# Performance work log

Measured on AMD Instinct MI355X. Metric: run time of the kernel, lower is better.

The kernel has to match this reference:

```python
import jax, jax.numpy as jnp
import numpy as np

D_MODEL = 1024
NUM_HEADS = 16
D_HEAD = D_MODEL // NUM_HEADS
BATCH, SEQ, MEM = 2, 1024, 1024
TOT = SEQ + MEM


def setup_inputs() -> dict:
    key = jax.random.key(0)
    ks = jax.random.split(key, 16)
    s = 0.02
    return {
        "x": jax.random.normal(ks[0], (BATCH, SEQ, D_MODEL), jnp.float32),
        "mem": jax.random.normal(ks[1], (BATCH, MEM, D_MODEL), jnp.float32),
        "mask": jnp.zeros((1, 1, SEQ, TOT), jnp.float32),
        "rel_enc": jax.random.normal(ks[2], (TOT, D_MODEL), jnp.float32),
        "Wq": jax.random.normal(ks[3], (D_MODEL, D_MODEL), jnp.float32) * s,
        "bq": jnp.zeros((D_MODEL,), jnp.float32),
        "Wke": jax.random.normal(ks[4], (D_MODEL, D_MODEL), jnp.float32) * s,
        "bke": jnp.zeros((D_MODEL,), jnp.float32),
        "Wkr": jax.random.normal(ks[5], (D_MODEL, D_MODEL), jnp.float32) * s,
        "bkr": jnp.zeros((D_MODEL,), jnp.float32),
        "Wv": jax.random.normal(ks[6], (D_MODEL, D_MODEL), jnp.float32) * s,
        "bv": jnp.zeros((D_MODEL,), jnp.float32),
        "Wo": jax.random.normal(ks[7], (D_MODEL, D_MODEL), jnp.float32) * s,
        "bo": jnp.zeros((D_MODEL,), jnp.float32),
    }


def _split_heads(t, b):
    # (b, s, d_model) -> (b, h, s, d_head)
    return t.reshape(b, -1, NUM_HEADS, D_HEAD).transpose(0, 2, 1, 3)


def _rel_enc_shift(arr):
    # arr: (b, h, l, m) -> Transformer-XL shift trick
    b, h, l, m = arr.shape
    arr = jnp.concatenate([arr, jnp.zeros((b, h, l, 1), arr.dtype)], axis=-1)
    arr = arr.reshape(b, h, l * (m + 1))
    return arr[:, :, l - 1:-1].reshape(b, h, l, m)


def reference(x, mem, mask, rel_enc, Wq, bq, Wke, bke, Wkr, bkr, Wv, bv, Wo, bo):
    b, s, _ = x.shape
    x_tilde = jnp.concatenate([mem, x], axis=1)  # (b, tot, d)
    q = _split_heads(x @ Wq + bq, b)             # (b, h, s, dh)
    k = _split_heads(x_tilde @ Wke + bke, b)     # (b, h, tot, dh)
    v = _split_heads(x_tilde @ Wv + bv, b)       # (b, h, tot, dh)
    A = jnp.einsum("bhsd,bhtd->bhst", q, k)      # content scores
    Q = (rel_enc @ Wkr + bkr).reshape(-1, NUM_HEADS, D_HEAD).transpose(1, 0, 2)  # (h, tot, dh)
    B_hat = jnp.einsum("bhsd,htd->bhst", q, Q)
    B = _rel_enc_shift(B_hat)                    # relative-position scores
    scores = (A + B) / jnp.sqrt(jnp.float32(D_HEAD)) + mask * -1e9
    w = jax.nn.softmax(scores, axis=-1)
    out = jnp.einsum("bhst,bhtd->bhsd", w, v)
    out = out.transpose(0, 2, 1, 3).reshape(b, s, D_MODEL)
    return out @ Wo + bo
```

## Files before the change

kernel.cpp:

```cpp
#include <hip/hip_runtime.h>

typedef unsigned short ushort;
typedef unsigned int uint;
typedef __attribute__((ext_vector_type(8))) short short8;
typedef __attribute__((ext_vector_type(4))) float float4v;

#define D_MODEL 1024
#define NH 16
#define DH 64
#define BATCH 2
#define SEQ 1024
#define MEMLEN 1024
#define TOT 2048
#define BROW 2056
#define PLN (1024 * BROW)

__device__ __forceinline__ float b2f(ushort u) {
  return __uint_as_float(((uint)u) << 16);
}
__device__ __forceinline__ ushort f2b(float f) {
  uint i = __float_as_uint(f);
  uint r = (i + 0x7fffu + ((i >> 16) & 1u)) >> 16;
  return (ushort)r;
}
__device__ __forceinline__ void gld16(const ushort* g, ushort* l) {
  __builtin_amdgcn_global_load_lds(
      (const __attribute__((address_space(1))) void*)g,
      (__attribute__((address_space(3))) void*)l, 16, 0, 0);
}

__global__ __launch_bounds__(256) void preproc_kernel(
    const float* __restrict__ x, const float* __restrict__ mem,
    const float* __restrict__ rel, const float* __restrict__ mask,
    ushort* __restrict__ xt, ushort* __restrict__ xb,
    ushort* __restrict__ relb, ushort* __restrict__ maskb) {
  const int bid = blockIdx.x;
  if (bid < 2048) {
    int idx = bid * 256 + threadIdx.x;
    int row = idx >> 7;
    int c8 = (idx & 127) << 3;
    int b = row >> 11;
    int i = row & 2047;
    const float* src = (i < MEMLEN) ? &mem[((b << 10) + i) * D_MODEL]
                                    : &x[((b << 10) + (i - MEMLEN)) * D_MODEL];
    float4 f0 = *(const float4*)(&src[c8]);
    float4 f1 = *(const float4*)(&src[c8 + 4]);
    ushort u[8] = {f2b(f0.x), f2b(f0.y), f2b(f0.z), f2b(f0.w),
                   f2b(f1.x), f2b(f1.y), f2b(f1.z), f2b(f1.w)};
    *(uint4*)(&xt[row * D_MODEL + c8]) = *(const uint4*)u;
    if (i >= MEMLEN)
      *(uint4*)(&xb[((b << 10) + (i - MEMLEN)) * D_MODEL + c8]) =
          *(const uint4*)u;
  } else if (bid < 3072) {
    int idx = (bid - 2048) * 256 + threadIdx.x;
    int base = idx << 3;
    float4 f0 = *(const float4*)(&rel[base]);
    float4 f1 = *(const float4*)(&rel[base + 4]);
    ushort u[8] = {f2b(f0.x), f2b(f0.y), f2b(f0.z), f2b(f0.w),
                   f2b(f1.x), f2b(f1.y), f2b(f1.z), f2b(f1.w)};
    *(uint4*)(&relb[base]) = *(const uint4*)u;
  } else {
    int idx = (bid - 3072) * 256 + threadIdx.x;
    int base = idx << 3;
    float4 f0 = *(const float4*)(&mask[base]);
    float4 f1 = *(const float4*)(&mask[base + 4]);
    ushort u[8] = {f2b(f0.x * -1e9f), f2b(f0.y * -1e9f), f2b(f0.z * -1e9f),
                   f2b(f0.w * -1e9f), f2b(f1.x * -1e9f), f2b(f1.y * -1e9f),
                   f2b(f1.z * -1e9f), f2b(f1.w * -1e9f)};
    *(uint4*)(&maskb[base]) = *(const uint4*)u;
  }
}

__global__ __launch_bounds__(256) void transpose_cvt5_kernel(
    const float* __restrict__ W0, const float* __restrict__ W1,
    const float* __restrict__ W2, const float* __restrict__ W3,
    const float* __restrict__ W4, ushort* __restrict__ T0,
    ushort* __restrict__ T1, ushort* __restrict__ T2, ushort* __restrict__ T3,
    ushort* __restrict__ T4) {
  __shared__ ushort tle[32][33];
  const float* W;
  ushort* T;
  switch (blockIdx.z) {
    case 0: W = W0; T = T0; break;
    case 1: W = W1; T = T1; break;
    case 2: W = W2; T = T2; break;
    case 3: W = W3; T = T3; break;
    default: W = W4; T = T4; break;
  }
  const int bx = blockIdx.x * 32, by = blockIdx.y * 32;
  const int tx = threadIdx.x & 31, ty = threadIdx.x >> 5;
#pragma unroll
  for (int j = 0; j < 32; j += 8)
    tle[ty + j][tx] = f2b(W[(by + ty + j) * 1024 + bx + tx]);
  __syncthreads();
#pragma unroll
  for (int j = 0; j < 32; j += 8)
    T[(bx + ty + j) * 1024 + by + tx] = tle[tx][ty + j];
}

__global__ __launch_bounds__(256) void gemm_fused_kernel(
    const ushort* __restrict__ xt, const ushort* __restrict__ xbrel,
    const ushort* __restrict__ WkeT, const ushort* __restrict__ WqT,
    const ushort* __restrict__ WkrT, const float* __restrict__ bke,
    const float* __restrict__ bv, const float* __restrict__ bq,
    const float* __restrict__ bkr, ushort* __restrict__ kv,
    ushort* __restrict__ qr) {
  __shared__ ushort As[128 * 32];
  __shared__ ushort Bs[128 * 32];
  const int bid = blockIdx.x;
  const bool seg0 = (bid < 512);
  const ushort* A;
  const ushort* BT;
  int m0, n0;
  if (seg0) {
    m0 = (bid & 31) * 128;
    n0 = (bid >> 5) * 128;
    A = xt;
    BT = WkeT;
  } else {
    int g = bid - 512;
    m0 = (g & 31) * 128;
    n0 = (g >> 5) * 128;
    A = xbrel;
    BT = (m0 < 2048) ? WqT : WkrT;
  }
  const int tid = threadIdx.x;
  const int w = tid >> 6, lane = tid & 63, m15 = lane & 15, q4 = lane >> 4;
  const int wm = w & 1, wn = w >> 1;
  float4v acc[4][4] = {};
  const int c0 = tid, c1 = tid + 256;
  const int r0 = c0 >> 2, u0 = (c0 & 3) * 8;
  const int r1 = c1 >> 2, u1 = (c1 & 3) * 8;

  for (int kk = 0; kk < 1024; kk += 32) {
    __syncthreads();
    gld16(&A[(m0 + r0) * 1024 + kk + u0], &As[c0 * 8]);
    gld16(&A[(m0 + r1) * 1024 + kk + u1], &As[c1 * 8]);
    gld16(&BT[(n0 + r0) * 1024 + kk + u0], &Bs[c0 * 8]);
    gld16(&BT[(n0 + r1) * 1024 + kk + u1], &Bs[c1 * 8]);
    __syncthreads();
    short8 af[4], bf[4];
#pragma unroll
    for (int i = 0; i < 4; ++i)
      af[i] = *(const short8*)(&As[(wm * 64 + i * 16 + m15) * 32 + q4 * 8]);
#pragma unroll
    for (int j = 0; j < 4; ++j)
      bf[j] = *(const short8*)(&Bs[(wn * 64 + j * 16 + m15) * 32 + q4 * 8]);
#pragma unroll
    for (int i = 0; i < 4; ++i)
#pragma unroll
      for (int j = 0; j < 4; ++j)
        acc[i][j] =
            __builtin_amdgcn_mfma_f32_16x16x32_bf16(af[i], bf[j], acc[i][j], 0, 0, 0);
  }
#pragma unroll
  for (int j = 0; j < 4; ++j) {
    int col = n0 + wn * 64 + j * 16 + m15;
    if (seg0) {
      if (col < 1024) {
        float bb = bke[col];
#pragma unroll
        for (int i = 0; i < 4; ++i) {
          int rowb = m0 + wm * 64 + i * 16 + q4 * 4;
#pragma unroll
          for (int r = 0; r < 4; ++r)
            kv[(rowb + r) * 2048 + col] = f2b((acc[i][j][r] + bb) * 0.125f);
        }
      } else {
        float bb = bv[col - 1024];
#pragma unroll
        for (int i = 0; i < 4; ++i) {
          int rowb = m0 + wm * 64 + i * 16 + q4 * 4;
          int dg = ((rowb >> 11) << 10) + (col - 1024);
          size_t prow = (size_t)(dg * 2 + ((rowb >> 10) & 1)) * 2048 + 1024 +
                        (rowb & 1023);
          uint lo = (uint)f2b(acc[i][j][0] + bb) |
                    ((uint)f2b(acc[i][j][1] + bb) << 16);
          uint hi = (uint)f2b(acc[i][j][2] + bb) |
                    ((uint)f2b(acc[i][j][3] + bb) << 16);
          *(uint2*)(&kv[prow]) = make_uint2(lo, hi);
        }
      }
    } else {
      float bb = (m0 < 2048) ? bq[col] : bkr[col];
      float sc = (m0 < 2048) ? 1.0f : 0.125f;
#pragma unroll
      for (int i = 0; i < 4; ++i) {
        int rowb = m0 + wm * 64 + i * 16 + q4 * 4;
#pragma unroll
        for (int r = 0; r < 4; ++r)
          qr[(rowb + r) * 1024 + col] = f2b((acc[i][j][r] + bb) * sc);
      }
    }
  }
}

template <int EPI>
__global__ __launch_bounds__(256) void gemm64_kernel(
    const ushort* __restrict__ A, const ushort* __restrict__ BT,
    const float* __restrict__ bias, void* __restrict__ Cout, int M, int N,
    int K) {
  __shared__ ushort As[64 * 32];
  __shared__ ushort Bs[128 * 32];
  const int m0 = blockIdx.x * 64, n0 = blockIdx.y * 128;
  const int tid = threadIdx.x;
  const int w = tid >> 6, lane = tid & 63, m15 = lane & 15, q4 = lane >> 4;
  float4v acc[4][2] = {};
  const int ra = tid >> 2, ua = (tid & 3) * 8;
  const int c0 = tid, c1 = tid + 256;
  const int rb0 = c0 >> 2, ub0 = (c0 & 3) * 8;
  const int rb1 = c1 >> 2, ub1 = (c1 & 3) * 8;

  for (int kk = 0; kk < K; kk += 32) {
    __syncthreads();
    gld16(&A[(m0 + ra) * K + kk + ua], &As[tid * 8]);
    gld16(&BT[(n0 + rb0) * K + kk + ub0], &Bs[c0 * 8]);
    gld16(&BT[(n0 + rb1) * K + kk + ub1], &Bs[c1 * 8]);
    __syncthreads();
    short8 bf[2];
#pragma unroll
    for (int j = 0; j < 2; ++j)
      bf[j] = *(const short8*)(&Bs[(w * 32 + j * 16 + m15) * 32 + q4 * 8]);
#pragma unroll
    for (int i = 0; i < 4; ++i) {
      short8 af = *(const short8*)(&As[(i * 16 + m15) * 32 + q4 * 8]);
#pragma unroll
      for (int j = 0; j < 2; ++j)
        acc[i][j] =
            __builtin_amdgcn_mfma_f32_16x16x32_bf16(af, bf[j], acc[i][j], 0, 0, 0);
    }
  }
#pragma unroll
  for (int j = 0; j < 2; ++j) {
    int col = n0 + w * 32 + j * 16 + m15;
    float bv = bias[col];
#pragma unroll
    for (int i = 0; i < 4; ++i) {
      int rowb = m0 + i * 16 + q4 * 4;
#pragma unroll
      for (int r = 0; r < 4; ++r) {
        float v = acc[i][j][r] + bv;
        if (EPI == 1)
          ((float*)Cout)[(rowb + r) * N + col] = v;
        else
          ((ushort*)Cout)[(rowb + r) * N + col] = f2b(v);
      }
    }
  }
}

__global__ __launch_bounds__(256) void bhat_kernel(
    const ushort* __restrict__ q, const ushort* __restrict__ Qrb,
    const ushort* __restrict__ maskb, ushort* __restrict__ Bh) {
  __shared__ ushort As[2 * 128 * 32];
  __shared__ ushort Bs[2 * 128 * 32];
  const int bs0 = blockIdx.x * 128, u0 = blockIdx.y * 128, h = blockIdx.z;
  const int tid = threadIdx.x;
  const int w = tid >> 6, lane = tid & 63, m15 = lane & 15, q4 = lane >> 4;
  const int wm = w & 1, wn = w >> 1;

#pragma unroll
  for (int c = 0; c < 4; ++c) {
    int unit = c * 256 + tid;
    int row = (unit >> 2) & 127, kh = unit >> 9, cu = unit & 3;
    gld16(&q[(bs0 + row) * 1024 + (h << 6) + kh * 32 + cu * 8], &As[unit * 8]);
    gld16(&Qrb[(u0 + row) * 1024 + (h << 6) + kh * 32 + cu * 8], &Bs[unit * 8]);
  }
  __syncthreads();

  float4v acc[4][4] = {};
#pragma unroll
  for (int kh = 0; kh < 2; ++kh) {
    short8 af[4], bf[4];
#pragma unroll
    for (int i = 0; i < 4; ++i)
      af[i] = *(const short8*)(&As[kh * 4096 + (wm * 64 + i * 16 + m15) * 32 + q4 * 8]);
#pragma unroll
    for (int j = 0; j < 4; ++j)
      bf[j] = *(const short8*)(&Bs[kh * 4096 + (wn * 64 + j * 16 + m15) * 32 + q4 * 8]);
#pragma unroll
    for (int i = 0; i < 4; ++i)
#pragma unroll
      for (int j = 0; j < 4; ++j)
        acc[i][j] =
            __builtin_amdgcn_mfma_f32_16x16x32_bf16(af[i], bf[j], acc[i][j], 0, 0, 0);
  }
  const int b = bs0 >> 10;
  const int s0loc = bs0 & 1023;
  const int pbase = ((b << 4) + h) * PLN;
#pragma unroll
  for (int j = 0; j < 4; ++j) {
    int u = u0 + wn * 64 + j * 16 + m15;
#pragma unroll
    for (int i = 0; i < 4; ++i) {
      int spb = s0loc + wm * 64 + i * 16 + q4 * 4;
#pragma unroll
      for (int r = 0; r < 4; ++r) {
        int sp = spb + r;
        bool selA = (u >= 1023 - sp);
        int mrow = selA ? sp : (sp > 0 ? sp - 1 : 0);
        int mcol = selA ? (u + sp - 1023) : (u + sp + 1025);
        float mval = b2f(maskb[mrow * 2048 + mcol]);
        Bh[pbase + sp * BROW + ((sp + 1) & 7) + u] = f2b(acc[i][j][r] + mval);
      }
    }
  }
}

__global__ __launch_bounds__(256) void attn_kernel(
    const ushort* __restrict__ qb, const ushort* __restrict__ kv,
    const ushort* __restrict__ Bh, const ushort* __restrict__ maskb,
    ushort* __restrict__ attn) {
  __shared__ ushort Ks[4][32 * 64];
  __shared__ ushort Vs[4][64 * 32];
  __shared__ ushort BA[4][64 * 32];
  __shared__ ushort BB[4][64 * 32];
  __shared__ ushort Pp[4][16 * 36];

  const int tid = threadIdx.x;
  const int w = tid >> 6, lane = tid & 63, m15 = lane & 15, q4 = lane >> 4;
  const int s0 = blockIdx.x * 64;
  const int h = blockIdx.y, b = blockIdx.z;
  const int s_l = q4 * 4;
  const int sw0 = s0 + w * 16;

  const ushort* qp = &qb[((b << 10) + sw0 + m15) * 1024 + (h << 6) + q4 * 8];
  const short8 af0 = *(const short8*)qp;
  const short8 af1 = *(const short8*)(qp + 32);

  const ushort* kvb = &kv[((size_t)(b << 11) * 2048) + (h << 6)];
  const size_t vbase = ((size_t)((b << 10) + (h << 6)) * 2) * 2048;
  const int pbase = ((b << 4) + h) * PLN;
  ushort* pw = &Pp[w][0];

  float dm[4];
  int diagT[4];
#pragma unroll
  for (int i = 0; i < 4; ++i) {
    int s = sw0 + s_l + i;
    diagT[i] = s + 1025;
    dm[i] = (diagT[i] <= 2047) ? b2f(maskb[s * 2048 + diagT[i]]) : 0.f;
  }
  asm volatile("s_waitcnt vmcnt(0)" ::: "memory");
  __builtin_amdgcn_sched_barrier(0);

  const int rK = tid >> 3, cK = tid & 7;
  const int rV = tid >> 2, cV = tid & 3;
  const int rB = tid >> 2, cB = tid & 3;
  const int sB = s0 + rB;
  const int offA_l = pbase + sB * BROW + ((sB + 1) & 7) - sB + 1023;
  const int offB_l = pbase + (sB + 1) * BROW + ((sB + 2) & 7) - sB - 1026;
  const int segK = cK ^ (rK & 7);
  const int segV = cV ^ ((rV >> 2) & 3);
  const int segB = cB ^ ((rB >> 2) & 3);

  float lsum4[4] = {0.f, 0.f, 0.f, 0.f};
  float4v oacc[4] = {};

#define STAGE(c, sl)                                                          \
  {                                                                           \
    const int t0_ = (c) * 32;                                                 \
    gld16(&kvb[(size_t)(t0_ + rK) * 2048 + segK * 8], &Ks[sl][tid * 8]);      \
    gld16(&kv[vbase + ((size_t)rV * 2 + (t0_ >> 10)) * 2048 + 1024 +          \
              (t0_ & 1023) + segV * 8],                                       \
          &Vs[sl][tid * 8]);                                                  \
    int t8_ = t0_ + segB * 8;                                                 \
    int offa_ = (t8_ <= sB + 1025) ? offA_l : offB_l;                         \
    gld16(&Bh[offa_ + t8_], &BA[sl][tid * 8]);                                \
    bool str_ = (t0_ + 31 >= s0 + 1018) && (t0_ <= s0 + 1088);                \
    int offb_ = str_ ? offB_l : offa_;                                        \
    gld16(&Bh[offb_ + t8_], &BB[sl][tid * 8]);                                \
  }

#define WAITV(n)                                                              \
  __builtin_amdgcn_sched_barrier(0);                                          \
  asm volatile("s_waitcnt vmcnt(" #n ")" ::: "memory");                       \
  __builtin_amdgcn_sched_barrier(0);                                          \
  __builtin_amdgcn_s_barrier();

  auto compute = [&](int c, int sl) {
    const int t0 = c * 32;
    short8 Kf[2][2];
#pragma unroll
    for (int nt = 0; nt < 2; ++nt)
#pragma unroll
      for (int ko = 0; ko < 2; ++ko)
        Kf[nt][ko] = *(const short8*)(&Ks[sl][(nt * 16 + m15) * 64 +
                                              (((q4 + 4 * ko) ^ (m15 & 7)) << 3)]);
    short8 Vf[4];
#pragma unroll
    for (int nd = 0; nd < 4; ++nd) {
      int d = nd * 16 + m15;
      Vf[nd] = *(const short8*)(&Vs[sl][d * 32 + ((q4 ^ ((d >> 2) & 3)) << 3)]);
    }
    float4v a0 = {}, a1 = {};
    a0 = __builtin_amdgcn_mfma_f32_16x16x32_bf16(af0, Kf[0][0], a0, 0, 0, 0);
    a0 = __builtin_amdgcn_mfma_f32_16x16x32_bf16(af1, Kf[0][1], a0, 0, 0, 0);
    a1 = __builtin_amdgcn_mfma_f32_16x16x32_bf16(af0, Kf[1][0], a1, 0, 0, 0);
    a1 = __builtin_amdgcn_mfma_f32_16x16x32_bf16(af1, Kf[1][1], a1, 0, 0, 0);
    const bool strad = (t0 + 31 >= s0 + 1018) && (t0 <= s0 + 1088);
    if (!strad) {
#pragma unroll
      for (int nt = 0; nt < 2; ++nt)
#pragma unroll
        for (int i = 0; i < 4; ++i) {
          int rr = (w << 4) + s_l + i;
          int cc = nt * 16 + m15;
          ushort bu = BA[sl][rr * 32 + (((cc >> 3) ^ q4) << 3) + (cc & 7)];
          float a = nt ? a1[i] : a0[i];
          float p = __expf(a + b2f(bu));
          lsum4[i] += p;
          pw[(s_l + i) * 36 + cc] = f2b(p);
        }
    } else {
#pragma unroll
      for (int nt = 0; nt < 2; ++nt)
#pragma unroll
        for (int i = 0; i < 4; ++i) {
          int rr = (w << 4) + s_l + i;
          int cc = nt * 16 + m15;
          int t = t0 + cc;
          int li = rr * 32 + (((cc >> 3) ^ q4) << 3) + (cc & 7);
          int s = sw0 + s_l + i;
          float va = b2f(BA[sl][li]);
          float vb = b2f(BB[sl][li]);
          int t8 = t & ~7;
          float bval = (t == diagT[i])
                           ? dm[i]
                           : ((t > diagT[i] && t8 <= s + 1025) ? vb : va);
          float a = nt ? a1[i] : a0[i];
          float p = __expf(a + bval);
          lsum4[i] += p;
          pw[(s_l + i) * 36 + cc] = f2b(p);
        }
    }
    short8 pfr = *(const short8*)(&pw[m15 * 36 + q4 * 8]);
#pragma unroll
    for (int nd = 0; nd < 4; ++nd)
      oacc[nd] =
          __builtin_amdgcn_mfma_f32_16x16x32_bf16(pfr, Vf[nd], oacc[nd], 0, 0, 0);
  };

  STAGE(0, 0);
  STAGE(1, 1);
  STAGE(2, 2);
  for (int j = 0; j < 15; ++j) {
    const int c = j * 4;
    STAGE(c + 3, 3); WAITV(12); compute(c, 0); __builtin_amdgcn_s_barrier();
    STAGE(c + 4, 0); WAITV(12); compute(c + 1, 1); __builtin_amdgcn_s_barrier();
    STAGE(c + 5, 1); WAITV(12); compute(c + 2, 2); __builtin_amdgcn_s_barrier();
    STAGE(c + 6, 2); WAITV(12); compute(c + 3, 3); __builtin_amdgcn_s_barrier();
  }
  STAGE(63, 3); WAITV(12); compute(60, 0); __builtin_amdgcn_s_barrier();
  WAITV(8);  compute(61, 1); __builtin_amdgcn_s_barrier();
  WAITV(4);  compute(62, 2); __builtin_amdgcn_s_barrier();
  WAITV(0);  compute(63, 3);

#pragma unroll
  for (int i = 0; i < 4; ++i) {
    float v = lsum4[i];
    v += __shfl_xor(v, 1, 64);
    v += __shfl_xor(v, 2, 64);
    v += __shfl_xor(v, 4, 64);
    v += __shfl_xor(v, 8, 64);
    lsum4[i] = v;
  }
#pragma unroll
  for (int nd = 0; nd < 4; ++nd)
#pragma unroll
    for (int i = 0; i < 4; ++i)
      attn[((b << 10) + sw0 + s_l + i) * 1024 + (h << 6) + nd * 16 + m15] =
          f2b(oacc[nd][i] / lsum4[i]);
#undef STAGE
#undef WAITV
}

extern "C" void kernel_launch(void* const* d_in, const int* in_sizes, int n_in,
                              void* d_out, int out_size, void* d_ws,
                              size_t ws_size, hipStream_t stream) {
  const float* x = (const float*)d_in[0];
  const float* mem = (const float*)d_in[1];
  const float* mask = (const float*)d_in[2];
  const float* rel = (const float*)d_in[3];
  const float* Wq = (const float*)d_in[4];
  const float* bq = (const float*)d_in[5];
  const float* Wke = (const float*)d_in[6];
  const float* bke = (const float*)d_in[7];
  const float* Wkr = (const float*)d_in[8];
  const float* bkr = (const float*)d_in[9];
  const float* Wv = (const float*)d_in[10];
  const float* bv = (const float*)d_in[11];
  const float* Wo = (const float*)d_in[12];
  const float* bo = (const float*)d_in[13];
  float* out = (float*)d_out;

  ushort* ws = (ushort*)d_ws;
  ushort* xt = ws;
  ushort* xbrel = xt + 4096 * 1024;
  ushort* WqT = xbrel + 4096 * 1024;
  ushort* WkeT = WqT + 1024 * 1024;
  ushort* WvT = WkeT + 1024 * 1024;
  ushort* WkrT = WvT + 1024 * 1024;
  ushort* WoT = WkrT + 1024 * 1024;
  ushort* kv = WoT + 1024 * 1024;
  ushort* qr = kv + 4096 * 2048;
  ushort* attn = qr + 4096 * 1024;
  ushort* maskb = attn + 2048 * 1024;
  ushort* Bh = maskb + 1024 * 2048;
  ushort* relb = xbrel + 2048 * 1024;
  ushort* Qrb = qr + 2048 * 1024;

  preproc_kernel<<<4096, 256, 0, stream>>>(x, mem, rel, mask, xt, xbrel, relb,
                                           maskb);
  transpose_cvt5_kernel<<<dim3(32, 32, 5), 256, 0, stream>>>(
      Wq, Wke, Wkr, Wv, Wo, WqT, WkeT, WkrT, WvT, WoT);

  gemm_fused_kernel<<<768, 256, 0, stream>>>(xt, xbrel, WkeT, WqT, WkrT, bke,
                                             bv, bq, bkr, kv, qr);

  bhat_kernel<<<dim3(16, 16, 16), 256, 0, stream>>>(qr, Qrb, maskb, Bh);

  attn_kernel<<<dim3(16, NH, BATCH), 256, 0, stream>>>(qr, kv, Bh, maskb,
                                                       attn);

  gemm64_kernel<1><<<dim3(32, 8), 256, 0, stream>>>(attn, WoT, bo, out, 2048,
                                                    1024, 1024);
}
```

Baseline: 314.1 us.

## Split attention over key range into two halves and combine partials

The attention grid doubles so that each block processes half of the 2048 key positions, writing unnormalized fp32 partial outputs and row sums. A new combine kernel adds the two partials, normalizes them and converts to bf16 for the output GEMM. The second B-tile shared-memory stage is removed, and the rare straddle elements are read directly from global memory instead. This raises occupancy from 512 blocks to 1024, at the cost of extra fp32 traffic and one more launch. It depends on the softmax having no max subtraction, so the partial sums can simply be added.

New measurement: 328.8 us. 4.7% more time.

```diff
diff --git a/kernel.cpp b/kernel.cpp
--- a/kernel.cpp
+++ b/kernel.cpp
@@ -310,19 +310,20 @@
 __global__ __launch_bounds__(256) void attn_kernel(
     const ushort* __restrict__ qb, const ushort* __restrict__ kv,
     const ushort* __restrict__ Bh, const ushort* __restrict__ maskb,
-    ushort* __restrict__ attn) {
+    float* __restrict__ pO0, float* __restrict__ pO1, float* __restrict__ pL) {
   __shared__ ushort Ks[4][32 * 64];
   __shared__ ushort Vs[4][64 * 32];
   __shared__ ushort BA[4][64 * 32];
-  __shared__ ushort BB[4][64 * 32];
   __shared__ ushort Pp[4][16 * 36];
 
   const int tid = threadIdx.x;
   const int w = tid >> 6, lane = tid & 63, m15 = lane & 15, q4 = lane >> 4;
-  const int s0 = blockIdx.x * 64;
+  const int stile = blockIdx.x & 15, th = blockIdx.x >> 4;
+  const int s0 = stile * 64;
   const int h = blockIdx.y, b = blockIdx.z;
   const int s_l = q4 * 4;
   const int sw0 = s0 + w * 16;
+  const int tb = th * 1024;
 
   const ushort* qp = &qb[((b << 10) + sw0 + m15) * 1024 + (h << 6) + q4 * 8];
   const short8 af0 = *(const short8*)qp;
@@ -334,12 +335,10 @@
   ushort* pw = &Pp[w][0];
 
   float dm[4];
-  int diagT[4];
 #pragma unroll
   for (int i = 0; i < 4; ++i) {
     int s = sw0 + s_l + i;
-    diagT[i] = s + 1025;
-    dm[i] = (diagT[i] <= 2047) ? b2f(maskb[s * 2048 + diagT[i]]) : 0.f;
+    dm[i] = (s + 1025 <= 2047) ? b2f(maskb[s * 2048 + s + 1025]) : 0.f;
   }
   asm volatile("s_waitcnt vmcnt(0)" ::: "memory");
   __builtin_amdgcn_sched_barrier(0);
@@ -359,7 +358,7 @@
 
 #define STAGE(c, sl)                                                          \
   {                                                                           \
-    const int t0_ = (c) * 32;                                                 \
+    const int t0_ = tb + (c) * 32;                                            \
     gld16(&kvb[(size_t)(t0_ + rK) * 2048 + segK * 8], &Ks[sl][tid * 8]);      \
     gld16(&kv[vbase + ((size_t)rV * 2 + (t0_ >> 10)) * 2048 + 1024 +          \
               (t0_ & 1023) + segV * 8],                                       \
@@ -367,9 +366,6 @@
     int t8_ = t0_ + segB * 8;                                                 \
     int offa_ = (t8_ <= sB + 1025) ? offA_l : offB_l;                         \
     gld16(&Bh[offa_ + t8_], &BA[sl][tid * 8]);                                \
-    bool str_ = (t0_ + 31 >= s0 + 1018) && (t0_ <= s0 + 1088);                \
-    int offb_ = str_ ? offB_l : offa_;                                        \
-    gld16(&Bh[offb_ + t8_], &BB[sl][tid * 8]);                                \
   }
 
 #define WAITV(n)                                                              \
@@ -379,7 +375,7 @@
   __builtin_amdgcn_s_barrier();
 
   auto compute = [&](int c, int sl) {
-    const int t0 = c * 32;
+    const int t0 = tb + c * 32;
     short8 Kf[2][2];
 #pragma unroll
     for (int nt = 0; nt < 2; ++nt)
@@ -398,7 +394,7 @@
     a0 = __builtin_amdgcn_mfma_f32_16x16x32_bf16(af1, Kf[0][1], a0, 0, 0, 0);
     a1 = __builtin_amdgcn_mfma_f32_16x16x32_bf16(af0, Kf[1][0], a1, 0, 0, 0);
     a1 = __builtin_amdgcn_mfma_f32_16x16x32_bf16(af1, Kf[1][1], a1, 0, 0, 0);
-    const bool strad = (t0 + 31 >= s0 + 1018) && (t0 <= s0 + 1088);
+    const bool strad = (t0 + 31 >= s0 + 994) && (t0 <= s0 + 1096);
     if (!strad) {
 #pragma unroll
       for (int nt = 0; nt < 2; ++nt)
@@ -422,12 +418,15 @@
           int t = t0 + cc;
           int li = rr * 32 + (((cc >> 3) ^ q4) << 3) + (cc & 7);
           int s = sw0 + s_l + i;
-          float va = b2f(BA[sl][li]);
-          float vb = b2f(BB[sl][li]);
-          int t8 = t & ~7;
-          float bval = (t == diagT[i])
-                           ? dm[i]
-                           : ((t > diagT[i] && t8 <= s + 1025) ? vb : va);
+          float bval;
+          if (t == s + 1025) {
+            bval = dm[i];
+          } else if (t > s + 1025 && (t & ~7) <= s + 1025) {
+            int offBe = pbase + (s + 1) * BROW + ((s + 2) & 7) - s - 1026;
+            bval = b2f(Bh[offBe + t]);
+          } else {
+            bval = b2f(BA[sl][li]);
+          }
           float a = nt ? a1[i] : a0[i];
           float p = __expf(a + bval);
           lsum4[i] += p;
@@ -444,17 +443,17 @@
   STAGE(0, 0);
   STAGE(1, 1);
   STAGE(2, 2);
-  for (int j = 0; j < 15; ++j) {
+  for (int j = 0; j < 7; ++j) {
     const int c = j * 4;
-    STAGE(c + 3, 3); WAITV(12); compute(c, 0); __builtin_amdgcn_s_barrier();
-    STAGE(c + 4, 0); WAITV(12); compute(c + 1, 1); __builtin_amdgcn_s_barrier();
-    STAGE(c + 5, 1); WAITV(12); compute(c + 2, 2); __builtin_amdgcn_s_barrier();
-    STAGE(c + 6, 2); WAITV(12); compute(c + 3, 3); __builtin_amdgcn_s_barrier();
-  }
-  STAGE(63, 3); WAITV(12); compute(60, 0); __builtin_amdgcn_s_barrier();
-  WAITV(8);  compute(61, 1); __builtin_amdgcn_s_barrier();
-  WAITV(4);  compute(62, 2); __builtin_amdgcn_s_barrier();
-  WAITV(0);  compute(63, 3);
+    STAGE(c + 3, 3); WAITV(9); compute(c, 0); __builtin_amdgcn_s_barrier();
+    STAGE(c + 4, 0); WAITV(9); compute(c + 1, 1); __builtin_amdgcn_s_barrier();
+    STAGE(c + 5, 1); WAITV(9); compute(c + 2, 2); __builtin_amdgcn_s_barrier();
+    STAGE(c + 6, 2); WAITV(9); compute(c + 3, 3); __builtin_amdgcn_s_barrier();
+  }
+  STAGE(31, 3); WAITV(9); compute(28, 0); __builtin_amdgcn_s_barrier();
+  WAITV(6); compute(29, 1); __builtin_amdgcn_s_barrier();
+  WAITV(3); compute(30, 2); __builtin_amdgcn_s_barrier();
+  WAITV(0); compute(31, 3);
 
 #pragma unroll
   for (int i = 0; i < 4; ++i) {
@@ -465,14 +464,38 @@
     v += __shfl_xor(v, 8, 64);
     lsum4[i] = v;
   }
+  float* pO = th ? pO1 : pO0;
 #pragma unroll
   for (int nd = 0; nd < 4; ++nd)
 #pragma unroll
     for (int i = 0; i < 4; ++i)
-      attn[((b << 10) + sw0 + s_l + i) * 1024 + (h << 6) + nd * 16 + m15] =
-          f2b(oacc[nd][i] / lsum4[i]);
+      pO[(size_t)((b << 10) + sw0 + s_l + i) * 1024 + (h << 6) + nd * 16 +
+         m15] = oacc[nd][i];
+  if (m15 == 0)
+#pragma unroll
+    for (int i = 0; i < 4; ++i)
+      pL[((((th << 1) | b) << 4) | h) * 1024 + sw0 + s_l + i] = lsum4[i];
 #undef STAGE
 #undef WAITV
+}
+
+__global__ __launch_bounds__(256) void combine_kernel(
+    const float* __restrict__ pO0, const float* __restrict__ pO1,
+    const float* __restrict__ pL, ushort* __restrict__ attnb) {
+  int idx = blockIdx.x * 256 + threadIdx.x;
+  int e4 = idx << 2;
+  int b = e4 >> 20;
+  int s = (e4 >> 10) & 1023;
+  int d = e4 & 1023;
+  int h = d >> 6;
+  float l0 = pL[((b << 4) | h) * 1024 + s];
+  float l1 = pL[(((2 + b) << 4) | h) * 1024 + s];
+  float inv = 1.0f / (l0 + l1);
+  float4 v0 = ((const float4*)pO0)[idx];
+  float4 v1 = ((const float4*)pO1)[idx];
+  ushort u[4] = {f2b((v0.x + v1.x) * inv), f2b((v0.y + v1.y) * inv),
+                 f2b((v0.z + v1.z) * inv), f2b((v0.w + v1.w) * inv)};
+  *(uint2*)(&attnb[e4]) = *(const uint2*)u;
 }
 
 extern "C" void kernel_launch(void* const* d_in, const int* in_sizes, int n_in,
@@ -504,11 +527,14 @@
   ushort* WoT = WkrT + 1024 * 1024;
   ushort* kv = WoT + 1024 * 1024;
   ushort* qr = kv + 4096 * 2048;
-  ushort* attn = qr + 4096 * 1024;
-  ushort* maskb = attn + 2048 * 1024;
+  ushort* attnb = qr + 4096 * 1024;
+  ushort* maskb = attnb + 2048 * 1024;
   ushort* Bh = maskb + 1024 * 2048;
   ushort* relb = xbrel + 2048 * 1024;
   ushort* Qrb = qr + 2048 * 1024;
+  float* pO0 = (float*)xt;
+  float* pO1 = (float*)xbrel;
+  float* pL = (float*)(Bh + (size_t)32 * PLN + 4096);
 
   preproc_kernel<<<4096, 256, 0, stream>>>(x, mem, rel, mask, xt, xbrel, relb,
                                            maskb);
@@ -520,9 +546,11 @@
 
   bhat_kernel<<<dim3(16, 16, 16), 256, 0, stream>>>(qr, Qrb, maskb, Bh);
 
-  attn_kernel<<<dim3(16, NH, BATCH), 256, 0, stream>>>(qr, kv, Bh, maskb,
-                                                       attn);
-
-  gemm64_kernel<1><<<dim3(32, 8), 256, 0, stream>>>(attn, WoT, bo, out, 2048,
+  attn_kernel<<<dim3(32, NH, BATCH), 256, 0, stream>>>(qr, kv, Bh, maskb, pO0,
+                                                       pO1, pL);
+
+  combine_kernel<<<2048, 256, 0, stream>>>(pO0, pO1, pL, attnb);
+
+  gemm64_kernel<1><<<dim3(32, 8), 256, 0, stream>>>(attnb, WoT, bo, out, 2048,
                                                     1024, 1024);
 }
```
